# Kernel tuning notes

Hardware: AMD Instinct MI355X
Metric: run time of the kernel (lower is better)

The kernel has to match this reference:

```python
import jax, jax.numpy as jnp
import numpy as np

NUM_CATES = 3000
HIDDEN = 64
N_GROUPS = 4
N_LAYERS = 2
HOP_NUM = 4
ALPHA = 0.15
EPS = 1e-5
B, L = 256, 50


def setup_inputs() -> dict:
    key = jax.random.key(0)
    ks = jax.random.split(key, 12)
    cate_list = jax.random.randint(ks[0], (B, L), 0, NUM_CATES)
    # sparse-ish binary adjacency with self loops (avg degree ~30)
    adj = (jax.random.uniform(ks[1], (NUM_CATES, NUM_CATES)) < 0.01).astype(jnp.float32)
    adj = jnp.maximum(adj, jnp.eye(NUM_CATES, dtype=jnp.float32))
    kaiming = (2.0 / HIDDEN) ** 0.5
    emb = jax.random.normal(ks[2], (NUM_CATES, HIDDEN)) * kaiming   # embedding_cates.weight
    Wq = jax.random.normal(ks[3], (N_LAYERS, HIDDEN, HIDDEN)) * HIDDEN ** -0.5
    Wk = jax.random.normal(ks[4], (N_LAYERS, HIDDEN, HIDDEN)) * HIDDEN ** -0.5
    Wv = jax.random.normal(ks[5], (N_LAYERS, HIDDEN, HIDDEN)) * HIDDEN ** -0.5
    Wg = jax.random.normal(ks[6], (HIDDEN, N_GROUPS)) * kaiming     # group_func
    bg = jnp.zeros((N_GROUPS,), jnp.float32)
    Wp = jax.random.normal(ks[7], (NUM_CATES, 1)) * (2.0 / NUM_CATES) ** 0.5  # group_pool_func
    bp = jnp.zeros((1,), jnp.float32)
    gamma = jnp.ones((HIDDEN,), jnp.float32)                        # custom BatchNorm scale
    beta = jnp.zeros((HIDDEN,), jnp.float32)                        # custom BatchNorm shift
    return {"cate_list": cate_list, "adj": adj, "emb": emb, "Wq": Wq, "Wk": Wk,
            "Wv": Wv, "Wg": Wg, "bg": bg, "Wp": Wp, "bp": bp, "gamma": gamma, "beta": beta}


def _magna_layer(h, adj, Wq, Wk, Wv):
    # graph attention diffusion (MAGNA): masked attention + hop_num PPR-style diffusion
    q = h @ Wq
    k = h @ Wk
    v = h @ Wv
    scores = (q @ k.T) / jnp.sqrt(jnp.float32(HIDDEN))          # [N, N]
    scores = jnp.where(adj > 0, scores, jnp.float32(-1e9))
    A = jax.nn.softmax(scores, axis=-1)
    z = v
    for _ in range(HOP_NUM):
        z = (1.0 - ALPHA) * (A @ z) + ALPHA * v
    return h + z                                                 # residual


def reference(cate_list, adj, emb, Wq, Wk, Wv, Wg, bg, Wp, bp, gamma, beta):
    h = emb
    for l in range(N_LAYERS):
        h = _magna_layer(h, adj, Wq[l], Wk[l], Wv[l])
    graph = h                                                    # [N, H]
    score_cluster = jax.nn.softmax(graph @ Wg + bg, axis=1)      # [N, G]
    # sub_graph[g, n, h] = score[n, g] * graph[n, h]
    sub_graph = score_cluster.T[:, :, None] * graph[None]        # [G, N, H]
    # per-user gather (vectorized index_select over batch)
    seq_emb = jnp.moveaxis(sub_graph[:, cate_list, :], 1, 0)     # [B, G, L, H]
    mask = (cate_list == 0)[:, None, :, None]                    # [B, 1, L, 1]
    seq_emb = jnp.where(mask, jnp.float32(0.0), seq_emb)
    # custom BatchNorm: normalize sub_graph with per-user stats from seq_emb
    mean = seq_emb.mean(axis=(1, 2), keepdims=True)              # [B, 1, 1, H]
    var = seq_emb.var(axis=(1, 2), keepdims=True)
    user_sub_graph = (sub_graph[None] - mean) / jnp.sqrt(var + EPS) * gamma + beta  # [B, G, N, H]
    user_sub_graph = jnp.swapaxes(user_sub_graph, 3, 2)          # [B, G, H, N]
    out = user_sub_graph @ Wp + bp                               # [B, G, H, 1]  (dropout = identity, eval)
    return out[..., 0]                                           # squeeze -> [B, G, H]
```

## Files before the change

kernel.cpp:

```cpp
#include <hip/hip_runtime.h>

#define NC 3000
#define NP 3072
#define CAP 64
#define HD 64
#define NG 4
#define LQ 50
#define NB 256
#define NQ4 750
#define SBST (NG * HD + 1)
#define NSBC 8
#define NBLK 256
#define TPB 768
#define WPB 12
#define NREP 32
#define ROOT (NBLK - 1)

__device__ __forceinline__ void stg(float* p, float v) {
  __hip_atomic_store(p, v, __ATOMIC_RELAXED, __HIP_MEMORY_SCOPE_AGENT);
}
__device__ __forceinline__ void stf(unsigned* p, unsigned v) {
  __hip_atomic_store(p, v, __ATOMIC_RELAXED, __HIP_MEMORY_SCOPE_AGENT);
}
__device__ __forceinline__ unsigned ldf(const unsigned* p) {
  return __hip_atomic_load(p, __ATOMIC_RELAXED, __HIP_MEMORY_SCOPE_AGENT);
}

__device__ __forceinline__ void gridbar(unsigned* __restrict__ slot,
                                        unsigned* __restrict__ rep, unsigned phase) {
  __syncthreads();
  const int tid = threadIdx.x;
  if (blockIdx.x == ROOT) {
    if (tid < 64) {
      if (tid == 0) stf(&slot[ROOT], phase);
      bool d0 = false, d1 = false, d2 = false, d3 = false;
      for (;;) {
        if (!d0) d0 = (ldf(&slot[tid]) >= phase);
        if (!d1) d1 = (ldf(&slot[tid + 64]) >= phase);
        if (!d2) d2 = (ldf(&slot[tid + 128]) >= phase);
        if (!d3) d3 = (ldf(&slot[tid + 192]) >= phase);
        if (__all((int)(d0 && d1 && d2 && d3))) break;
      }
      if (tid < NREP) stf(&rep[tid * 16], phase);
    }
    __syncthreads();
  } else {
    if (tid == 0) {
      stf(&slot[blockIdx.x], phase);
      while (ldf(&rep[(blockIdx.x & (NREP - 1)) * 16]) < phase) {}
    }
    __syncthreads();
  }
  asm volatile("" ::: "memory");
}

__device__ __forceinline__ float hopz(const float* __restrict__ zin, const int2* scvw,
                                      int d, int lane, float vown) {
  float acc = 0.f;
  const int dro = (d + 7) & ~7;
  for (int e = 0; e < dro; e += 8) {
    int2 a0 = scvw[e + 0], a1 = scvw[e + 1], a2 = scvw[e + 2], a3 = scvw[e + 3];
    int2 a4 = scvw[e + 4], a5 = scvw[e + 5], a6 = scvw[e + 6], a7 = scvw[e + 7];
    float z0 = zin[a0.x * HD + lane], z1 = zin[a1.x * HD + lane];
    float z2 = zin[a2.x * HD + lane], z3 = zin[a3.x * HD + lane];
    float z4 = zin[a4.x * HD + lane], z5 = zin[a5.x * HD + lane];
    float z6 = zin[a6.x * HD + lane], z7 = zin[a7.x * HD + lane];
    acc += __int_as_float(a0.y) * z0 + __int_as_float(a1.y) * z1
         + __int_as_float(a2.y) * z2 + __int_as_float(a3.y) * z3;
    acc += __int_as_float(a4.y) * z4 + __int_as_float(a5.y) * z5
         + __int_as_float(a6.y) * z6 + __int_as_float(a7.y) * z7;
  }
  return 0.85f * acc + 0.15f * vown;
}

__device__ __forceinline__ void qkv3(float h, const float* __restrict__ Wq,
                                     const float* __restrict__ Wk, const float* __restrict__ Wv,
                                     int lane, float& aq, float& ak, float& av) {
  aq = 0.f; ak = 0.f; av = 0.f;
#pragma unroll 16
  for (int f = 0; f < HD; ++f) {
    float hv = __shfl(h, f);
    aq += hv * Wq[f * HD + lane];
    ak += hv * Wk[f * HD + lane];
    av += hv * Wv[f * HD + lane];
  }
}

__device__ __forceinline__ void score_hop(const float* __restrict__ kbuf,
                                          const float* __restrict__ vsrc, float qreg, int creg,
                                          int d, int lane, float vown,
                                          float* __restrict__ zout, int row, int2* scvw) {
  float acc = 0.f;
  const float4* kr = reinterpret_cast<const float4*>(kbuf + creg * HD);
#pragma unroll
  for (int i = 0; i < 16; ++i) {
    float4 k4 = kr[i];
    acc += __shfl(qreg, 4 * i + 0) * k4.x;
    acc += __shfl(qreg, 4 * i + 1) * k4.y;
    acc += __shfl(qreg, 4 * i + 2) * k4.z;
    acc += __shfl(qreg, 4 * i + 3) * k4.w;
  }
  float e = (lane < d) ? __expf(acc * 0.125f) : 0.f;
  float s = e;
#pragma unroll
  for (int off = 1; off < 64; off <<= 1) s += __shfl_xor(s, off);
  float vreg = (s > 0.f) ? e / s : 0.f;
  scvw[lane] = make_int2(creg, __float_as_int(vreg));
  float hacc = hopz(vsrc, scvw, d, lane, vown);
  stg(zout + row * HD + lane, hacc);
}

__global__ __launch_bounds__(1024) void k_init(unsigned* __restrict__ slot,
                                               unsigned* __restrict__ rep,
                                               float* __restrict__ Sbp) {
  const int t = threadIdx.x;
  if (t < NBLK) stf(&slot[t], 0u);
  for (int i = t; i < NREP * 16; i += 1024) stf(&rep[i], 0u);
  for (int i = t; i < NSBC * SBST; i += 1024)
    __hip_atomic_store(&Sbp[i], 0.f, __ATOMIC_RELAXED, __HIP_MEMORY_SCOPE_AGENT);
}

__global__ __launch_bounds__(TPB, 1) void k_mega(
    const int* __restrict__ cate, const float* __restrict__ adj, const float* __restrict__ emb,
    const float* __restrict__ Wq, const float* __restrict__ Wk, const float* __restrict__ Wv,
    const float* __restrict__ Wg, const float* __restrict__ bg, const float* __restrict__ Wp,
    const float* __restrict__ bp, const float* __restrict__ gamma, const float* __restrict__ beta,
    float* __restrict__ out, float* __restrict__ kf, float* __restrict__ vf,
    float* __restrict__ kf2, float* __restrict__ vf2,
    float* __restrict__ z1, float* __restrict__ z2, float* __restrict__ z3,
    float* __restrict__ z5, float* __restrict__ z6, float* __restrict__ z7,
    float* __restrict__ hf, float* __restrict__ s2, float* __restrict__ Sbp,
    unsigned* __restrict__ slot, unsigned* __restrict__ rep) {
  const int tid = threadIdx.x, lane = tid & 63, wave = tid >> 6;
  const int blk = blockIdx.x;
  const int row = blk * WPB + wave;
  const bool inC = (row < NC);

  __shared__ int2 scv[WPB][CAP];
  __shared__ float Sl[NG * HD];
  __shared__ float Wl[WPB];
  __shared__ int cs[LQ];
  __shared__ float red[2 * WPB][HD];

  scv[wave][lane] = make_int2(0, 0);
  int d = 0;
  if (inC) {
    const float4* arow = reinterpret_cast<const float4*>(adj + (size_t)row * NC);
    const unsigned long long mlane = (1ull << lane) - 1ull;
    int base = 0;
#pragma unroll 3
    for (int g = 0; g < 12; ++g) {
      int idx = g * 64 + lane;
      float4 a4 = (idx < NQ4) ? arow[idx] : make_float4(0.f, 0.f, 0.f, 0.f);
      unsigned long long b0 = __ballot(a4.x != 0.f);
      unsigned long long b1 = __ballot(a4.y != 0.f);
      unsigned long long b2 = __ballot(a4.z != 0.f);
      unsigned long long b3 = __ballot(a4.w != 0.f);
      if (a4.x != 0.f) { int s = base + __popcll(b0 & mlane); if (s < CAP) scv[wave][s].x = 4 * idx + 0; }
      base += __popcll(b0);
      if (a4.y != 0.f) { int s = base + __popcll(b1 & mlane); if (s < CAP) scv[wave][s].x = 4 * idx + 1; }
      base += __popcll(b1);
      if (a4.z != 0.f) { int s = base + __popcll(b2 & mlane); if (s < CAP) scv[wave][s].x = 4 * idx + 2; }
      base += __popcll(b2);
      if (a4.w != 0.f) { int s = base + __popcll(b3 & mlane); if (s < CAP) scv[wave][s].x = 4 * idx + 3; }
      base += __popcll(b3);
    }
    d = (base < CAP) ? base : CAP;
  }
  const int creg = scv[wave][lane].x;
  int2* scvw = &scv[wave][0];
  float qreg = 0.f, vown = 0.f;
  if (inC) {
    float hreg = emb[row * HD + lane];
    float aq, ak, av;
    qkv3(hreg, Wq, Wk, Wv, lane, aq, ak, av);
    stg(kf + row * HD + lane, ak);
    stg(vf + row * HD + lane, av);
    qreg = aq;
    vown = av;
  }
  gridbar(slot, rep, 1);

  if (inC) score_hop(kf, vf, qreg, creg, d, lane, vown, z1, row, scvw);
  gridbar(slot, rep, 2);
  if (inC) stg(z2 + row * HD + lane, hopz(z1, scvw, d, lane, vown));
  gridbar(slot, rep, 3);
  if (inC) stg(z3 + row * HD + lane, hopz(z2, scvw, d, lane, vown));
  gridbar(slot, rep, 4);
  float h1 = 0.f;
  if (inC) {
    float z = hopz(z3, scvw, d, lane, vown);
    h1 = emb[row * HD + lane] + z;
    float aq, ak, av;
    qkv3(h1, Wq + HD * HD, Wk + HD * HD, Wv + HD * HD, lane, aq, ak, av);
    stg(kf2 + row * HD + lane, ak);
    stg(vf2 + row * HD + lane, av);
    qreg = aq; vown = av;
  }
  gridbar(slot, rep, 5);
  if (inC) score_hop(kf2, vf2, qreg, creg, d, lane, vown, z5, row, scvw);
  gridbar(slot, rep, 6);
  if (inC) stg(z6 + row * HD + lane, hopz(z5, scvw, d, lane, vown));
  gridbar(slot, rep, 7);
  if (inC) stg(z7 + row * HD + lane, hopz(z6, scvw, d, lane, vown));
  gridbar(slot, rep, 8);
  if (tid < NG * HD) Sl[tid] = 0.f;
  if (tid < WPB) Wl[tid] = 0.f;
  __syncthreads();
  if (inC) {
    float z = hopz(z7, scvw, d, lane, vown);
    float h = h1 + z;
    stg(hf + row * HD + lane, h);
    float4 wg = *reinterpret_cast<const float4*>(Wg + lane * NG);
    float a0 = h * wg.x, a1 = h * wg.y, a2 = h * wg.z, a3 = h * wg.w;
#pragma unroll
    for (int off = 1; off < 64; off <<= 1) {
      a0 += __shfl_xor(a0, off); a1 += __shfl_xor(a1, off);
      a2 += __shfl_xor(a2, off); a3 += __shfl_xor(a3, off);
    }
    float lg0 = a0 + bg[0], lg1 = a1 + bg[1], lg2 = a2 + bg[2], lg3 = a3 + bg[3];
    float mx = fmaxf(fmaxf(lg0, lg1), fmaxf(lg2, lg3));
    float e0 = __expf(lg0 - mx), e1 = __expf(lg1 - mx), e2 = __expf(lg2 - mx), e3 = __expf(lg3 - mx);
    float inv = 1.f / (e0 + e1 + e2 + e3);
    float p0 = e0 * inv, p1 = e1 * inv, p2 = e2 * inv, p3 = e3 * inv;
    if (lane == 0) stg(s2 + row, p0 * p0 + p1 * p1 + p2 * p2 + p3 * p3);
    float w = Wp[row];
    atomicAdd(&Sl[0 * HD + lane], p0 * w * h);
    atomicAdd(&Sl[1 * HD + lane], p1 * w * h);
    atomicAdd(&Sl[2 * HD + lane], p2 * w * h);
    atomicAdd(&Sl[3 * HD + lane], p3 * w * h);
    if (lane == 0) Wl[wave] = w;
  }
  __syncthreads();
  if (blk * WPB < NC) {
    float* Sc = Sbp + (blk & (NSBC - 1)) * SBST;
    if (tid < NG * HD) atomicAdd(&Sc[tid], Sl[tid]);
    if (tid == 0) {
      float ws = 0.f;
#pragma unroll
      for (int i = 0; i < WPB; ++i) ws += Wl[i];
      atomicAdd(&Sc[NG * HD], ws);
    }
  }
  gridbar(slot, rep, 9);
  if (blk < NB) {
    if (tid < LQ) cs[tid] = cate[blk * LQ + tid];
    __syncthreads();
    float msum = 0.f, qsum = 0.f;
    for (int l = wave; l < LQ; l += WPB) {
      int c = cs[l];
      if (c != 0) {
        float gv = hf[c * HD + lane];
        msum += gv;
        qsum += s2[c] * gv * gv;
      }
    }
    red[wave][lane] = msum;
    red[WPB + wave][lane] = qsum;
    __syncthreads();
    if (wave == 0) {
      msum = 0.f; qsum = 0.f;
#pragma unroll
      for (int i = 0; i < WPB; ++i) { msum += red[i][lane]; qsum += red[WPB + i][lane]; }
      const float cntf = 1.f / (NG * LQ);
      float mean = msum * cntf;
      float var = fmaxf(qsum * cntf - mean * mean, 0.f);
      float invs = rsqrtf(var + 1e-5f);
      float gam = gamma[lane], bet = beta[lane], bpv = bp[0];
      float wsum = 0.f;
#pragma unroll
      for (int i = 0; i < NSBC; ++i) wsum += Sbp[i * SBST + NG * HD];
#pragma unroll
      for (int g = 0; g < NG; ++g) {
        float sg = 0.f;
#pragma unroll
        for (int i = 0; i < NSBC; ++i) sg += Sbp[i * SBST + g * HD + lane];
        out[blk * (NG * HD) + g * HD + lane] = invs * gam * (sg - mean * wsum) + bet * wsum + bpv;
      }
    }
  }
}

extern "C" void kernel_launch(void* const* d_in, const int* in_sizes, int n_in,
                              void* d_out, int out_size, void* d_ws, size_t ws_size,
                              hipStream_t stream) {
  const int* cate = (const int*)d_in[0];
  const float* adj = (const float*)d_in[1];
  const float* emb = (const float*)d_in[2];
  const float* Wq = (const float*)d_in[3];
  const float* Wk = (const float*)d_in[4];
  const float* Wv = (const float*)d_in[5];
  const float* Wg = (const float*)d_in[6];
  const float* bg = (const float*)d_in[7];
  const float* Wp = (const float*)d_in[8];
  const float* bp = (const float*)d_in[9];
  const float* gamma = (const float*)d_in[10];
  const float* beta = (const float*)d_in[11];
  float* out = (float*)d_out;

  char* p = (char*)d_ws;
  auto carve = [&](size_t bytes) { char* r = p; p += (bytes + 255) & ~(size_t)255; return r; };
  float* kf = (float*)carve((size_t)NP * HD * 4);
  float* vf = (float*)carve((size_t)NP * HD * 4);
  float* kf2 = (float*)carve((size_t)NP * HD * 4);
  float* vf2 = (float*)carve((size_t)NP * HD * 4);
  float* z1 = (float*)carve((size_t)NP * HD * 4);
  float* z2 = (float*)carve((size_t)NP * HD * 4);
  float* z3 = (float*)carve((size_t)NP * HD * 4);
  float* z5 = (float*)carve((size_t)NP * HD * 4);
  float* z6 = (float*)carve((size_t)NP * HD * 4);
  float* z7 = (float*)carve((size_t)NP * HD * 4);
  float* hf = (float*)carve((size_t)NP * HD * 4);
  float* s2 = (float*)carve((size_t)NP * 4);
  float* Sbp = (float*)carve((size_t)NSBC * SBST * 4);
  unsigned* slot = (unsigned*)carve((size_t)NBLK * 4);
  unsigned* rep = (unsigned*)carve((size_t)NREP * 16 * 4);

  k_init<<<1, 1024, 0, stream>>>(slot, rep, Sbp);
  k_mega<<<NBLK, TPB, 0, stream>>>(cate, adj, emb, Wq, Wk, Wv, Wg, bg, Wp, bp, gamma, beta,
                                   out, kf, vf, kf2, vf2, z1, z2, z3, z5, z6, z7,
                                   hf, s2, Sbp, slot, rep);
}
```

Measured before the change: 163.5 us.

## Replace flat grid barrier with hierarchical per-XCD barrier using L2-local counters

Grid barriers 2 through 9 become two-level. Blocks first count arrivals on a per-XCD atomic counter scoped to the workgroup, so it resolves in that XCD's L2, and spin on an L2 release word. Only one leader per XCD signals the root block across dies. This cuts the number of cross-XCD agent-scope stores and polls per barrier. It relies on reading HW_REG_XCC_ID, on inline sc0 loads, and on per-XCD block counts being known after the first barrier, which adds memory-ordering and coherence risk for data written through non-coherent L2s.

```diff
diff --git a/kernel.cpp b/kernel.cpp
--- a/kernel.cpp
+++ b/kernel.cpp
@@ -14,6 +14,7 @@
 #define TPB 768
 #define WPB 12
 #define NREP 32
+#define NXCD 8
 #define ROOT (NBLK - 1)
 
 __device__ __forceinline__ void stg(float* p, float v) {
@@ -25,32 +26,76 @@
 __device__ __forceinline__ unsigned ldf(const unsigned* p) {
   return __hip_atomic_load(p, __ATOMIC_RELAXED, __HIP_MEMORY_SCOPE_AGENT);
 }
-
-__device__ __forceinline__ void gridbar(unsigned* __restrict__ slot,
-                                        unsigned* __restrict__ rep, unsigned phase) {
+__device__ __forceinline__ unsigned l2add1(unsigned* p) {
+  return __hip_atomic_fetch_add(p, 1u, __ATOMIC_RELAXED, __HIP_MEMORY_SCOPE_WORKGROUP);
+}
+__device__ __forceinline__ unsigned l2read(const unsigned* p) {
+  unsigned out;
+  asm volatile("global_load_dword %0, %1, off sc0\n\ts_waitcnt vmcnt(0)"
+               : "=v"(out) : "v"(p) : "memory");
+  return out;
+}
+
+__device__ __forceinline__ void gridbar1(unsigned* __restrict__ gslot,
+                                         unsigned* __restrict__ rep) {
   __syncthreads();
   const int tid = threadIdx.x;
   if (blockIdx.x == ROOT) {
     if (tid < 64) {
-      if (tid == 0) stf(&slot[ROOT], phase);
+      if (tid == 0) stf(&gslot[ROOT], 1u);
       bool d0 = false, d1 = false, d2 = false, d3 = false;
       for (;;) {
-        if (!d0) d0 = (ldf(&slot[tid]) >= phase);
-        if (!d1) d1 = (ldf(&slot[tid + 64]) >= phase);
-        if (!d2) d2 = (ldf(&slot[tid + 128]) >= phase);
-        if (!d3) d3 = (ldf(&slot[tid + 192]) >= phase);
+        if (!d0) d0 = (ldf(&gslot[tid]) >= 1u);
+        if (!d1) d1 = (ldf(&gslot[tid + 64]) >= 1u);
+        if (!d2) d2 = (ldf(&gslot[tid + 128]) >= 1u);
+        if (!d3) d3 = (ldf(&gslot[tid + 192]) >= 1u);
         if (__all((int)(d0 && d1 && d2 && d3))) break;
       }
-      if (tid < NREP) stf(&rep[tid * 16], phase);
+      if (tid < NREP) stf(&rep[tid * 16], 1u);
     }
     __syncthreads();
   } else {
     if (tid == 0) {
-      stf(&slot[blockIdx.x], phase);
-      while (ldf(&rep[(blockIdx.x & (NREP - 1)) * 16]) < phase) {}
+      stf(&gslot[blockIdx.x], 1u);
+      while (ldf(&rep[(blockIdx.x & (NREP - 1)) * 16]) < 1u) {}
     }
     __syncthreads();
   }
+  asm volatile("" ::: "memory");
+}
+
+__device__ __forceinline__ void localbar(unsigned* __restrict__ xslot,
+                                         unsigned* __restrict__ rep,
+                                         unsigned* __restrict__ lcnt,
+                                         unsigned* __restrict__ lrel,
+                                         unsigned xcd, unsigned nx, unsigned i,
+                                         bool isRoot) {
+  __syncthreads();
+  const int tid = threadIdx.x;
+  if (isRoot && tid >= 64 && tid < 128) {
+    int l = tid - 64;
+    bool dn = (l >= NXCD);
+    for (;;) {
+      if (!dn) dn = (ldf(&xslot[l * 16]) >= i);
+      if (__all((int)dn)) break;
+    }
+    if (l < NXCD) stf(&rep[l * 16], i);
+  }
+  if (tid == 0) {
+    unsigned old = l2add1(&lcnt[xcd * 16]);
+    if (old == nx * (i - 1) - 1u) {
+      stf(&xslot[xcd * 16], i);
+      while (ldf(&rep[xcd * 16]) < i) {}
+      l2add1(&lrel[xcd * 16]);
+    } else {
+      unsigned it = 0;
+      for (;;) {
+        if (l2read(&lrel[xcd * 16]) >= i - 1u) break;
+        if (((++it) & 63u) == 0u && ldf(&rep[xcd * 16]) >= i) break;
+      }
+    }
+  }
+  __syncthreads();
   asm volatile("" ::: "memory");
 }
 
@@ -110,12 +155,14 @@
   stg(zout + row * HD + lane, hacc);
 }
 
-__global__ __launch_bounds__(1024) void k_init(unsigned* __restrict__ slot,
+__global__ __launch_bounds__(1024) void k_init(unsigned* __restrict__ gslot,
                                                unsigned* __restrict__ rep,
+                                               unsigned* __restrict__ xstate,
                                                float* __restrict__ Sbp) {
   const int t = threadIdx.x;
-  if (t < NBLK) stf(&slot[t], 0u);
+  if (t < NBLK) stf(&gslot[t], 0u);
   for (int i = t; i < NREP * 16; i += 1024) stf(&rep[i], 0u);
+  for (int i = t; i < 4 * NXCD * 16; i += 1024) stf(&xstate[i], 0u);
   for (int i = t; i < NSBC * SBST; i += 1024)
     __hip_atomic_store(&Sbp[i], 0.f, __ATOMIC_RELAXED, __HIP_MEMORY_SCOPE_AGENT);
 }
@@ -130,11 +177,21 @@
     float* __restrict__ z1, float* __restrict__ z2, float* __restrict__ z3,
     float* __restrict__ z5, float* __restrict__ z6, float* __restrict__ z7,
     float* __restrict__ hf, float* __restrict__ s2, float* __restrict__ Sbp,
-    unsigned* __restrict__ slot, unsigned* __restrict__ rep) {
+    unsigned* __restrict__ gslot, unsigned* __restrict__ rep, unsigned* __restrict__ xstate) {
   const int tid = threadIdx.x, lane = tid & 63, wave = tid >> 6;
   const int blk = blockIdx.x;
   const int row = blk * WPB + wave;
   const bool inC = (row < NC);
+  const bool isRoot = (blk == ROOT);
+
+  unsigned* xslot = xstate;
+  unsigned* lcnt = xstate + NXCD * 16;
+  unsigned* lrel = xstate + 2 * NXCD * 16;
+  unsigned* xcnt = xstate + 3 * NXCD * 16;
+
+  unsigned xcd;
+  asm volatile("s_getreg_b32 %0, hwreg(HW_REG_XCC_ID)" : "=s"(xcd));
+  xcd &= 7u;
 
   __shared__ int2 scv[WPB][CAP];
   __shared__ float Sl[NG * HD];
@@ -142,6 +199,8 @@
   __shared__ int cs[LQ];
   __shared__ float red[2 * WPB][HD];
 
+  if (tid == 0)
+    __hip_atomic_fetch_add(&xcnt[xcd * 16], 1u, __ATOMIC_RELAXED, __HIP_MEMORY_SCOPE_AGENT);
   scv[wave][lane] = make_int2(0, 0);
   int d = 0;
   if (inC) {
@@ -179,14 +238,16 @@
     qreg = aq;
     vown = av;
   }
-  gridbar(slot, rep, 1);
+  gridbar1(gslot, rep);
+  unsigned nx = 0;
+  if (tid == 0) nx = ldf(&xcnt[xcd * 16]);
 
   if (inC) score_hop(kf, vf, qreg, creg, d, lane, vown, z1, row, scvw);
-  gridbar(slot, rep, 2);
+  localbar(xslot, rep, lcnt, lrel, xcd, nx, 2, isRoot);
   if (inC) stg(z2 + row * HD + lane, hopz(z1, scvw, d, lane, vown));
-  gridbar(slot, rep, 3);
+  localbar(xslot, rep, lcnt, lrel, xcd, nx, 3, isRoot);
   if (inC) stg(z3 + row * HD + lane, hopz(z2, scvw, d, lane, vown));
-  gridbar(slot, rep, 4);
+  localbar(xslot, rep, lcnt, lrel, xcd, nx, 4, isRoot);
   float h1 = 0.f;
   if (inC) {
     float z = hopz(z3, scvw, d, lane, vown);
@@ -197,13 +258,13 @@
     stg(vf2 + row * HD + lane, av);
     qreg = aq; vown = av;
   }
-  gridbar(slot, rep, 5);
+  localbar(xslot, rep, lcnt, lrel, xcd, nx, 5, isRoot);
   if (inC) score_hop(kf2, vf2, qreg, creg, d, lane, vown, z5, row, scvw);
-  gridbar(slot, rep, 6);
+  localbar(xslot, rep, lcnt, lrel, xcd, nx, 6, isRoot);
   if (inC) stg(z6 + row * HD + lane, hopz(z5, scvw, d, lane, vown));
-  gridbar(slot, rep, 7);
+  localbar(xslot, rep, lcnt, lrel, xcd, nx, 7, isRoot);
   if (inC) stg(z7 + row * HD + lane, hopz(z6, scvw, d, lane, vown));
-  gridbar(slot, rep, 8);
+  localbar(xslot, rep, lcnt, lrel, xcd, nx, 8, isRoot);
   if (tid < NG * HD) Sl[tid] = 0.f;
   if (tid < WPB) Wl[tid] = 0.f;
   __syncthreads();
@@ -242,7 +303,7 @@
       atomicAdd(&Sc[NG * HD], ws);
     }
   }
-  gridbar(slot, rep, 9);
+  localbar(xslot, rep, lcnt, lrel, xcd, nx, 9, isRoot);
   if (blk < NB) {
     if (tid < LQ) cs[tid] = cate[blk * LQ + tid];
     __syncthreads();
@@ -313,11 +374,12 @@
   float* hf = (float*)carve((size_t)NP * HD * 4);
   float* s2 = (float*)carve((size_t)NP * 4);
   float* Sbp = (float*)carve((size_t)NSBC * SBST * 4);
-  unsigned* slot = (unsigned*)carve((size_t)NBLK * 4);
+  unsigned* gslot = (unsigned*)carve((size_t)NBLK * 4);
   unsigned* rep = (unsigned*)carve((size_t)NREP * 16 * 4);
-
-  k_init<<<1, 1024, 0, stream>>>(slot, rep, Sbp);
+  unsigned* xstate = (unsigned*)carve((size_t)4 * NXCD * 16 * 4);
+
+  k_init<<<1, 1024, 0, stream>>>(gslot, rep, xstate, Sbp);
   k_mega<<<NBLK, TPB, 0, stream>>>(cate, adj, emb, Wq, Wk, Wv, Wg, bg, Wp, bp, gamma, beta,
                                    out, kf, vf, kf2, vf2, z1, z2, z3, z5, z6, z7,
-                                   hf, s2, Sbp, slot, rep);
-}
+                                   hf, s2, Sbp, gslot, rep, xstate);
+}
```

Result: slower. 207.1 us (+26.6%).
